# Performance work log

Hardware: AMD Instinct MI355X
Metric: run time of the kernel (lower is better)

The kernel has to match this reference:

```python
import jax, jax.numpy as jnp
import numpy as np

B, S, D, H = 2, 2048, 2048, 16
HD = D // H  # 128, head_dim (even, as asserted)
MAX_POS = 2048


def setup_inputs() -> dict:
    key = jax.random.key(0)
    ks = jax.random.split(key, 5)
    x = jax.random.normal(ks[0], (B, S, D), jnp.float32)
    Wq = jax.random.normal(ks[1], (D, D), jnp.float32) * 0.02
    Wk = jax.random.normal(ks[2], (D, D), jnp.float32) * 0.02
    Wv = jax.random.normal(ks[3], (D, D), jnp.float32) * 0.02
    Wo = jax.random.normal(ks[4], (D, D), jnp.float32) * 0.02
    # standard RoPE tables: [MAX_POS, HD]
    inv_freq = 1.0 / (10000.0 ** (jnp.arange(0, HD, 2, dtype=jnp.float32) / HD))
    angles = jnp.arange(MAX_POS, dtype=jnp.float32)[:, None] * inv_freq  # [P, HD/2]
    emb = jnp.concatenate([angles, angles], axis=-1)  # [P, HD]
    cos_freqs = jnp.cos(emb)
    sin_freqs = jnp.sin(emb)
    position_ids = jnp.broadcast_to(jnp.arange(S, dtype=jnp.int32), (B, S))
    return {"x": x, "cos_freqs": cos_freqs, "sin_freqs": sin_freqs,
            "Wq": Wq, "Wk": Wk, "Wv": Wv, "Wo": Wo,
            "position_ids": position_ids}


def _apply_rope(t, cos, sin, position_ids):
    # t: [b, s, h, hd]; cos/sin: [P, hd]; position_ids: [b, s]
    c = cos[position_ids][:, :, None, :]  # [b, s, 1, hd]
    s_ = sin[position_ids][:, :, None, :]
    t1, t2 = jnp.split(t, 2, axis=-1)
    rot = jnp.concatenate([-t2, t1], axis=-1)  # rotate-half
    return t * c + rot * s_


def reference(x, cos_freqs, sin_freqs, Wq, Wk, Wv, Wo, position_ids):
    b, s, d = x.shape
    q = (x @ Wq).reshape(b, s, H, HD)
    k = (x @ Wk).reshape(b, s, H, HD)  # n_kv_heads == n_heads
    v = (x @ Wv).reshape(b, s, H, HD)
    q = _apply_rope(q, cos_freqs, sin_freqs, position_ids)
    k = _apply_rope(k, cos_freqs, sin_freqs, position_ids)
    # [b, h, s, hd]
    q_t = jnp.swapaxes(q, 1, 2)
    k_t = jnp.swapaxes(k, 1, 2)
    v_t = jnp.swapaxes(v, 1, 2)
    scale = 1.0 / jnp.sqrt(jnp.float32(HD))
    scores = jnp.einsum('bhsd,bhtd->bhst', q_t, k_t) * scale  # O(s^2) matrix
    causal = jnp.tril(jnp.ones((s, s), dtype=bool))
    scores = jnp.where(causal[None, None, :, :], scores, -1e9)
    weights = jax.nn.softmax(scores, axis=-1)
    out = jnp.einsum('bhst,bhtd->bhsd', weights, v_t)
    out = jnp.swapaxes(out, 1, 2).reshape(b, s, d)
    out = out @ Wo
    return (out, k, v)  # kv_cache is post-RoPE, pre-transpose as in original
```

## Files before the change

kernel.cpp:

```cpp
#include <hip/hip_runtime.h>
#include <hip/hip_bf16.h>

#define B_ 2
#define S_ 2048
#define D_ 2048
#define H_ 16
#define HD_ 128
#define M_ (B_*S_)
#define BSD ((size_t)B_*S_*D_)

typedef short bf16x8 __attribute__((ext_vector_type(8)));
typedef float floatx4 __attribute__((ext_vector_type(4)));
typedef __hip_bfloat16 bf16;

union cv8 { bf16 h[8]; uint4 u; bf16x8 v; };

__device__ inline cv8 cvt8(const float4 a, const float4 b) {
    cv8 c;
    c.h[0] = __float2bfloat16(a.x); c.h[1] = __float2bfloat16(a.y);
    c.h[2] = __float2bfloat16(a.z); c.h[3] = __float2bfloat16(a.w);
    c.h[4] = __float2bfloat16(b.x); c.h[5] = __float2bfloat16(b.y);
    c.h[6] = __float2bfloat16(b.z); c.h[7] = __float2bfloat16(b.w);
    return c;
}

__device__ __forceinline__ void gld16(const void* g, void* l) {
    __builtin_amdgcn_global_load_lds(
        (const __attribute__((address_space(1))) unsigned int*)g,
        (__attribute__((address_space(3))) unsigned int*)l,
        16, 0, 0);
}

__global__ __launch_bounds__(256) void transpose_w(
    const float* __restrict__ W, bf16* __restrict__ Wt, int N, int K)
{
    __shared__ float T[32][33];
    const int k0 = blockIdx.x * 32, n0 = blockIdx.y * 32;
    const int r = threadIdx.x >> 3, c4 = (threadIdx.x & 7) * 4;
    float4 v = *(const float4*)&W[(size_t)(k0 + r) * N + n0 + c4];
    T[r][c4+0] = v.x; T[r][c4+1] = v.y; T[r][c4+2] = v.z; T[r][c4+3] = v.w;
    __syncthreads();
    union { bf16 h[4]; uint2 u; } o;
    #pragma unroll
    for (int i = 0; i < 4; ++i) o.h[i] = __float2bfloat16(T[c4 + i][r]);
    *(uint2*)&Wt[(size_t)(n0 + r) * K + k0 + c4] = o.u;
}

__global__ __launch_bounds__(256) void transpose_w_s(
    const float* __restrict__ W, bf16* __restrict__ Wt, int N, int K)
{
    __shared__ float T[32][33];
    const int k0 = blockIdx.x * 32, n0 = blockIdx.y * 32;
    const int r = threadIdx.x >> 3, c4 = (threadIdx.x & 7) * 4;
    float4 v = *(const float4*)&W[(size_t)(k0 + r) * N + n0 + c4];
    T[r][c4+0] = v.x; T[r][c4+1] = v.y; T[r][c4+2] = v.z; T[r][c4+3] = v.w;
    __syncthreads();
    union { bf16 h[4]; uint2 u; } o;
    #pragma unroll
    for (int i = 0; i < 4; ++i) o.h[i] = __float2bfloat16(T[c4 + i][r]);
    const int n = n0 + r;
    size_t bo = (size_t)n * (size_t)K * 2 + ((unsigned)((k0 + c4) * 2) ^ ((n & 3) << 4));
    *(uint2*)((char*)Wt + bo) = o.u;
}

__global__ __launch_bounds__(256) void pack_bf16(
    const float* __restrict__ src, bf16* __restrict__ dst)
{
    const size_t i = ((size_t)blockIdx.x * 256 + threadIdx.x) * 8;
    cv8 c = cvt8(*(const float4*)(src + i), *(const float4*)(src + i + 4));
    size_t bo = i * 2;
    bo ^= (size_t)(((bo >> 12) & 3) << 4);
    *(uint4*)((char*)dst + bo) = c.u;
}

__global__ __launch_bounds__(256) void rope_pack_k(
    float* __restrict__ k, bf16* __restrict__ kbb,
    const float* __restrict__ cf, const float* __restrict__ sf,
    const int* __restrict__ pos)
{
    const int idx = blockIdx.x * 256 + threadIdx.x;
    const int dg = idx & 7;
    const int h  = (idx >> 3) & (H_-1);
    const int bs = idx >> 7;
    const int s  = bs & (S_-1);
    const int b  = bs >> 11;
    const int p  = pos[bs];
    const size_t base = (size_t)bs * D_ + h*HD_ + dg*8;
    float lo[8], hi[8], c1[8], s1[8], c2[8], s2[8];
    *(float4*)&lo[0] = *(const float4*)&k[base];
    *(float4*)&lo[4] = *(const float4*)&k[base + 4];
    *(float4*)&hi[0] = *(const float4*)&k[base + 64];
    *(float4*)&hi[4] = *(const float4*)&k[base + 68];
    const float* cp = cf + (size_t)p*HD_ + dg*8;
    const float* sp = sf + (size_t)p*HD_ + dg*8;
    *(float4*)&c1[0] = *(const float4*)cp;        *(float4*)&c1[4] = *(const float4*)(cp + 4);
    *(float4*)&s1[0] = *(const float4*)sp;        *(float4*)&s1[4] = *(const float4*)(sp + 4);
    *(float4*)&c2[0] = *(const float4*)(cp + 64); *(float4*)&c2[4] = *(const float4*)(cp + 68);
    *(float4*)&s2[0] = *(const float4*)(sp + 64); *(float4*)&s2[4] = *(const float4*)(sp + 68);
    float nl[8], nh[8];
    #pragma unroll
    for (int j = 0; j < 8; ++j) {
        nl[j] = lo[j]*c1[j] - hi[j]*s1[j];
        nh[j] = hi[j]*c2[j] + lo[j]*s2[j];
    }
    *(float4*)&k[base]      = *(float4*)&nl[0];
    *(float4*)&k[base + 4]  = *(float4*)&nl[4];
    *(float4*)&k[base + 64] = *(float4*)&nh[0];
    *(float4*)&k[base + 68] = *(float4*)&nh[4];
    cv8 clo, chi;
    #pragma unroll
    for (int j = 0; j < 8; ++j) {
        clo.h[j] = __float2bfloat16(nl[j]);
        chi.h[j] = __float2bfloat16(nh[j]);
    }
    const size_t rowb = ((size_t)(b*H_ + h)*S_ + s) * (size_t)(HD_*2);
    *(uint4*)((char*)kbb + rowb + ((dg*16)       ^ ((s & 7) << 4))) = clo.u;
    *(uint4*)((char*)kbb + rowb + (((dg+8)*16)   ^ ((s & 7) << 4))) = chi.u;
}

__global__ __launch_bounds__(256) void pack_vt(
    const float* __restrict__ src, bf16* __restrict__ dst)
{
    __shared__ float T[32][33];
    const int s0 = blockIdx.x * 32;
    const int d0 = blockIdx.y * 32;
    const int bh = blockIdx.z;
    const int b = bh >> 4, h = bh & (H_-1);
    const int r = threadIdx.x >> 3, c4 = (threadIdx.x & 7) * 4;
    float4 v = *(const float4*)&src[((size_t)(b*S_ + s0 + r)*H_ + h)*HD_ + d0 + c4];
    T[r][c4+0] = v.x; T[r][c4+1] = v.y; T[r][c4+2] = v.z; T[r][c4+3] = v.w;
    __syncthreads();
    union { bf16 h4[4]; uint2 u; } o;
    #pragma unroll
    for (int i = 0; i < 4; ++i) o.h4[i] = __float2bfloat16(T[c4 + i][r]);
    const int hd = d0 + r;
    size_t rowb = ((size_t)bh*HD_ + hd) * (size_t)(S_*2);
    size_t colb = (size_t)(s0 + c4) * 2;
    colb = (colb & ~(size_t)127) | (((unsigned)colb & 127u) ^ (unsigned)((hd & 7) << 4));
    *(uint2*)((char*)dst + rowb + colb) = o.u;
}

__global__ __launch_bounds__(256, 3) void gemm_bb2(
    const bf16* __restrict__ A, const bf16* __restrict__ Wt,
    float* __restrict__ C, int M, int N, int K)
{
    __shared__ __align__(16) bf16 As[128][32];
    __shared__ __align__(16) bf16 Bs[128][32];
    const int nwg = (int)(gridDim.x * gridDim.y);
    int id = (int)(blockIdx.y * gridDim.x + blockIdx.x);
    if ((nwg & 7) == 0) id = (id & 7) * (nwg >> 3) + (id >> 3);
    const int m0 = (id % (int)gridDim.x) * 128;
    const int n0 = (id / (int)gridDim.x) * 128;
    const int tid = threadIdx.x, lane = tid & 63, w = tid >> 6;
    const int quad = lane >> 4, l16 = lane & 15;
    const int wrow = (w >> 1) * 64, wcol = (w & 1) * 64;
    const size_t K2 = (size_t)K * 2;

    floatx4 acc[4][4] = {};

    const char* Ab = (const char*)A;
    const char* Bb = (const char*)Wt;
    char* AsB = (char*)&As[0][0];
    char* BsB = (char*)&Bs[0][0];
    const int srow = lane >> 2;
    const int scol = (lane & 3) * 16;

    for (int kt = 0; kt < K; kt += 32) {
        #pragma unroll
        for (int j = 0; j < 2; ++j) {
            const int row = w*32 + j*16 + srow;
            gld16(Ab + (size_t)(m0 + row)*K2 + (size_t)(kt*2) + scol,
                  AsB + w*2048 + j*1024);
            gld16(Bb + (size_t)(n0 + row)*K2 + (size_t)(kt*2) + scol,
                  BsB + w*2048 + j*1024);
        }
        __syncthreads();

        bf16x8 af[4], bfr[4];
        #pragma unroll
        for (int t = 0; t < 4; ++t) {
            const int ra = wrow + t*16 + l16;
            af[t]  = *(const bf16x8*)(AsB + ra*64 + ((quad*16) ^ ((ra & 3) << 4)));
            const int rb = wcol + t*16 + l16;
            bfr[t] = *(const bf16x8*)(BsB + rb*64 + ((quad*16) ^ ((rb & 3) << 4)));
        }
        #pragma unroll
        for (int mt = 0; mt < 4; ++mt)
            #pragma unroll
            for (int nt = 0; nt < 4; ++nt)
                acc[mt][nt] = __builtin_amdgcn_mfma_f32_16x16x32_bf16(
                    af[mt], bfr[nt], acc[mt][nt], 0, 0, 0);
        __syncthreads();
    }

    #pragma unroll
    for (int mt = 0; mt < 4; ++mt)
        #pragma unroll
        for (int nt = 0; nt < 4; ++nt)
            #pragma unroll
            for (int r = 0; r < 4; ++r)
                C[(size_t)(m0 + wrow + mt*16 + quad*4 + r) * N
                  + n0 + wcol + nt*16 + l16] = acc[mt][nt][r];
}

__global__ __launch_bounds__(256) void gemm_xw(
    const float* __restrict__ A, const bf16* __restrict__ Wt,
    float* __restrict__ C, int M, int N, int K)
{
    __shared__ __align__(16) bf16 As[128][40];
    __shared__ __align__(16) bf16 Bs[128][40];
    const int m0 = blockIdx.x * 128, n0 = blockIdx.y * 128;
    const int tid = threadIdx.x, lane = tid & 63, w = tid >> 6;
    const int quad = lane >> 4, l16 = lane & 15;
    const int wrow = (w >> 1) * 64, wcol = (w & 1) * 64;
    floatx4 acc[4][4] = {};
    const int arow = tid >> 2;
    const int acol = (tid & 3) * 8;
    for (int kt = 0; kt < K; kt += 32) {
        #pragma unroll
        for (int p = 0; p < 2; ++p) {
            const int r = p*64 + arow;
            const float* ap = &A[(size_t)(m0 + r) * K + kt + acol];
            cv8 ca = cvt8(*(const float4*)ap, *(const float4*)(ap + 4));
            *(uint4*)&As[r][acol] = ca.u;
            const bf16* bp = &Wt[(size_t)(n0 + r) * K + kt + acol];
            *(uint4*)&Bs[r][acol] = *(const uint4*)bp;
        }
        __syncthreads();
        bf16x8 af[4], bfr[4];
        #pragma unroll
        for (int t = 0; t < 4; ++t) {
            af[t]  = *(const bf16x8*)&As[wrow + t*16 + l16][quad*8];
            bfr[t] = *(const bf16x8*)&Bs[wcol + t*16 + l16][quad*8];
        }
        #pragma unroll
        for (int mt = 0; mt < 4; ++mt)
            #pragma unroll
            for (int nt = 0; nt < 4; ++nt)
                acc[mt][nt] = __builtin_amdgcn_mfma_f32_16x16x32_bf16(
                    af[mt], bfr[nt], acc[mt][nt], 0, 0, 0);
        __syncthreads();
    }
    #pragma unroll
    for (int mt = 0; mt < 4; ++mt)
        #pragma unroll
        for (int nt = 0; nt < 4; ++nt)
            #pragma unroll
            for (int r = 0; r < 4; ++r)
                C[(size_t)(m0 + wrow + mt*16 + quad*4 + r) * N
                  + n0 + wcol + nt*16 + l16] = acc[mt][nt][r];
}

__global__ __launch_bounds__(256) void gemm_f32(
    const float* __restrict__ A, const float* __restrict__ W,
    float* __restrict__ C, int M, int N, int K)
{
    __shared__ __align__(16) bf16 As[64][40];
    __shared__ __align__(16) bf16 Bs[64][40];
    const int m0 = blockIdx.x * 64, n0 = blockIdx.y * 64;
    const int tid = threadIdx.x, lane = tid & 63, w = tid >> 6;
    const int quad = lane >> 4, l16 = lane & 15;
    const int wrow = (w >> 1) * 32, wcol = (w & 1) * 32;
    floatx4 acc[2][2] = {};
    const int ar = tid >> 2, ac = (tid & 3) * 8;
    const int br = tid >> 3, bc = (tid & 7) * 8;
    for (int kt = 0; kt < K; kt += 32) {
        {
            const float* ap = &A[(size_t)(m0 + ar) * K + kt + ac];
            cv8 c = cvt8(*(const float4*)ap, *(const float4*)(ap + 4));
            *(uint4*)&As[ar][ac] = c.u;
        }
        {
            const float* wp = &W[(size_t)(kt + br) * N + n0 + bc];
            cv8 c = cvt8(*(const float4*)wp, *(const float4*)(wp + 4));
            #pragma unroll
            for (int i = 0; i < 8; ++i) Bs[bc + i][br] = c.h[i];
        }
        __syncthreads();
        bf16x8 af[2], bfr[2];
        #pragma unroll
        for (int t = 0; t < 2; ++t) {
            af[t]  = *(const bf16x8*)&As[wrow + t*16 + l16][quad*8];
            bfr[t] = *(const bf16x8*)&Bs[wcol + t*16 + l16][quad*8];
        }
        #pragma unroll
        for (int mt = 0; mt < 2; ++mt)
            #pragma unroll
            for (int nt = 0; nt < 2; ++nt)
                acc[mt][nt] = __builtin_amdgcn_mfma_f32_16x16x32_bf16(
                    af[mt], bfr[nt], acc[mt][nt], 0, 0, 0);
        __syncthreads();
    }
    #pragma unroll
    for (int mt = 0; mt < 2; ++mt)
        #pragma unroll
        for (int nt = 0; nt < 2; ++nt)
            #pragma unroll
            for (int r = 0; r < 4; ++r)
                C[(size_t)(m0 + wrow + mt*16 + quad*4 + r) * N
                  + n0 + wcol + nt*16 + l16] = acc[mt][nt][r];
}

__global__ __launch_bounds__(256) void rope_kernel(
    float* __restrict__ q, float* __restrict__ k,
    const float* __restrict__ cf, const float* __restrict__ sf,
    const int* __restrict__ pos)
{
    const int PAIRS = B_*S_*H_*(HD_/2);
    int idx = blockIdx.x * 256 + threadIdx.x;
    float* t = q;
    if (idx >= PAIRS) { t = k; idx -= PAIRS; }
    const int d  = idx & 63;
    const int h  = (idx >> 6) & (H_-1);
    const int bs = idx >> 10;
    const int p  = pos[bs];
    const float c1 = cf[p*HD_ + d],      s1 = sf[p*HD_ + d];
    const float c2 = cf[p*HD_ + d + 64], s2 = sf[p*HD_ + d + 64];
    const size_t base = (size_t)bs * D_ + h*HD_ + d;
    const float t1 = t[base], t2 = t[base + 64];
    t[base]      = t1*c1 - t2*s1;
    t[base + 64] = t2*c2 + t1*s2;
}

__global__ __launch_bounds__(256, 3) void flash_attn_v6(
    const float* __restrict__ qg, const bf16* __restrict__ kb,
    const bf16* __restrict__ vb, bf16* __restrict__ ob,
    const float* __restrict__ cf, const float* __restrict__ sf,
    const int* __restrict__ pos)
{
    __shared__ __align__(16) bf16 Ks[2][64][128];
    __shared__ __align__(16) bf16 Vt[128][64];

    const int qi = (int)gridDim.x - 1 - (int)blockIdx.x;
    const int q0 = qi * 64;
    const int bh = blockIdx.y;
    const int b = bh >> 4, h = bh & (H_-1);
    const int tid = threadIdx.x, lane = tid & 63, w = tid >> 6;
    const int quad = lane >> 4, l16 = lane & 15;

    const char* kbase = (const char*)(kb + (size_t)bh * S_ * HD_);
    const char* vbase = (const char*)(vb + (size_t)bh * HD_ * S_);
    char* ksd = (char*)&Ks[0][0][0];
    char* vtd = (char*)&Vt[0][0];

    const int klofs = w*4096;
    const int vrow0 = w*32 + (lane >> 3);
    const int vcb   = (lane & 7) * 16;

    #pragma unroll
    for (int j = 0; j < 4; ++j)
        gld16(kbase + klofs + j*1024 + lane*16, ksd + klofs + j*1024);

    const int qrow = q0 + w*16 + l16;
    const float* qptr = qg + ((size_t)(b*S_ + qrow))*D_ + h*HD_;
    float rq[4][8];
    #pragma unroll
    for (int c = 0; c < 4; ++c) {
        const float* qp = qptr + c*32 + quad*8;
        *(float4*)&rq[c][0] = *(const float4*)qp;
        *(float4*)&rq[c][4] = *(const float4*)(qp + 4);
    }
    const int p = pos[b*S_ + qrow];
    bf16x8 qf[4];
    #pragma unroll
    for (int c = 0; c < 4; ++c) {
        const float* cp = cf + (size_t)p*HD_ + c*32 + quad*8;
        const float* sp = sf + (size_t)p*HD_ + c*32 + quad*8;
        float cc[8], ss[8];
        *(float4*)&cc[0] = *(const float4*)cp; *(float4*)&cc[4] = *(const float4*)(cp+4);
        *(float4*)&ss[0] = *(const float4*)sp; *(float4*)&ss[4] = *(const float4*)(sp+4);
        cv8 cv;
        #pragma unroll
        for (int j = 0; j < 8; ++j) {
            const float o = (c < 2) ? rq[c][j]*cc[j] - rq[c^2][j]*ss[j]
                                    : rq[c][j]*cc[j] + rq[c^2][j]*ss[j];
            cv.h[j] = __float2bfloat16(o);
        }
        qf[c] = cv.v;
    }

    floatx4 acc_o[8] = {};
    float m_run = -30000.0f, l_run = 0.0f;
    const int qr_sm = q0 + w*16 + l16;
    const float SCL = 0.08838834764831845f;

    __syncthreads();

    for (int kt = 0; kt <= qi; ++kt) {
        const int cur = kt & 1;
        const char* ksb = ksd + cur*16384;

        if (kt < qi) {
            const char* ksrc = kbase + (size_t)(kt+1)*16384;
            char* kdst = ksd + (cur^1)*16384;
            #pragma unroll
            for (int j = 0; j < 4; ++j)
                gld16(ksrc + klofs + j*1024 + lane*16, kdst + klofs + j*1024);
        }
        {
            const char* vsrc = vbase + (size_t)kt*128;
            #pragma unroll
            for (int j = 0; j < 4; ++j)
                gld16(vsrc + (size_t)(vrow0 + j*8)*(S_*2) + vcb,
                      vtd + w*4096 + j*1024);
        }

        floatx4 sc[4] = {};
        __builtin_amdgcn_s_setprio(1);
        #pragma unroll
        for (int c = 0; c < 4; ++c)
            #pragma unroll
            for (int kc = 0; kc < 4; ++kc) {
                bf16x8 kf = *(const bf16x8*)(ksb + (c*16 + l16)*256
                              + ((kc*64 + quad*16) ^ ((l16 & 7) << 4)));
                sc[c] = __builtin_amdgcn_mfma_f32_16x16x32_bf16(kf, qf[kc], sc[c], 0, 0, 0);
            }
        __builtin_amdgcn_s_setprio(0);

        const int k0 = kt * 64;
        float pv[4][4], mt = -30000.0f;
        #pragma unroll
        for (int c = 0; c < 4; ++c)
            #pragma unroll
            for (int r = 0; r < 4; ++r) {
                const int kcol = k0 + c*16 + quad*4 + r;
                float s = sc[c][r] * SCL;
                if (kcol > qr_sm) s = -30000.0f;
                pv[c][r] = s;
                mt = fmaxf(mt, s);
            }
        mt = fmaxf(mt, __shfl_xor(mt, 16, 64));
        mt = fmaxf(mt, __shfl_xor(mt, 32, 64));
        const float mn = fmaxf(m_run, mt);
        const float alpha = __expf(m_run - mn);
        m_run = mn;
        float sum = 0.0f;
        #pragma unroll
        for (int c = 0; c < 4; ++c)
            #pragma unroll
            for (int r = 0; r < 4; ++r) {
                pv[c][r] = __expf(pv[c][r] - mn);
                sum += pv[c][r];
            }
        sum += __shfl_xor(sum, 16, 64);
        sum += __shfl_xor(sum, 32, 64);
        l_run = l_run * alpha + sum;

        float at[4];
        #pragma unroll
        for (int r = 0; r < 4; ++r) at[r] = __shfl(alpha, quad*4 + r, 64);
        #pragma unroll
        for (int n = 0; n < 8; ++n)
            #pragma unroll
            for (int r = 0; r < 4; ++r)
                acc_o[n][r] *= at[r];

        unsigned pk[4][2];
        #pragma unroll
        for (int c = 0; c < 4; ++c) {
            union { bf16 h2[2]; unsigned u; } a0, a1;
            a0.h2[0] = __float2bfloat16(pv[c][0]); a0.h2[1] = __float2bfloat16(pv[c][1]);
            a1.h2[0] = __float2bfloat16(pv[c][2]); a1.h2[1] = __float2bfloat16(pv[c][3]);
            pk[c][0] = a0.u; pk[c][1] = a1.u;
        }
        bf16x8 pf[2];
        #pragma unroll
        for (int kc2 = 0; kc2 < 2; ++kc2) {
            union { unsigned u[4]; bf16x8 v; } wv;
            #pragma unroll
            for (int u_ = 0; u_ < 4; ++u_) {
                const int sl = ((quad & 1)*2 + (u_ >> 1))*16 + l16;
                const unsigned w0 = __shfl(pk[kc2*2 + 0][u_ & 1], sl, 64);
                const unsigned w1 = __shfl(pk[kc2*2 + 1][u_ & 1], sl, 64);
                wv.u[u_] = (quad >> 1) ? w1 : w0;
            }
            pf[kc2] = wv.v;
        }

        __syncthreads();

        __builtin_amdgcn_s_setprio(1);
        #pragma unroll
        for (int n = 0; n < 8; ++n)
            #pragma unroll
            for (int kc2 = 0; kc2 < 2; ++kc2) {
                bf16x8 vf = *(const bf16x8*)(vtd + (n*16 + l16)*128
                               + ((kc2*64 + quad*16) ^ ((l16 & 7) << 4)));
                acc_o[n] = __builtin_amdgcn_mfma_f32_16x16x32_bf16(pf[kc2], vf, acc_o[n], 0, 0, 0);
            }
        __builtin_amdgcn_s_setprio(0);

        __syncthreads();
    }

    const float linv = 1.0f / l_run;
    float lt[4];
    #pragma unroll
    for (int r = 0; r < 4; ++r) lt[r] = __shfl(linv, quad*4 + r, 64);
    #pragma unroll
    for (int n = 0; n < 8; ++n)
        #pragma unroll
        for (int r = 0; r < 4; ++r) {
            const int qr = q0 + w*16 + quad*4 + r;
            size_t bo = ((((size_t)(b*S_ + qr))*D_ + h*HD_ + n*16 + l16) * 2)
                        ^ (size_t)(r << 4);
            *(bf16*)((char*)ob + bo) = __float2bfloat16(acc_o[n][r] * lt[r]);
        }
}

__global__ __launch_bounds__(256) void flash_attn(
    const float* qg, const float* __restrict__ kg,
    const float* __restrict__ vg, float* og)
{
    __shared__ __align__(16) bf16 Ks[64][136];
    __shared__ __align__(16) bf16 Vt[128][72];
    __shared__ __align__(16) bf16 Ps[4][16][72];

    const int qi = (int)gridDim.x - 1 - (int)blockIdx.x;
    const int q0 = qi * 64;
    const int bh = blockIdx.y;
    const int b = bh >> 4, h = bh & (H_-1);
    const int tid = threadIdx.x, lane = tid & 63, w = tid >> 6;
    const int quad = lane >> 4, l16 = lane & 15;

    const int qrow = q0 + w*16 + l16;
    const float* qptr = qg + ((size_t)(b*S_ + qrow)*H_ + h)*HD_;
    bf16x8 qf[4];
    #pragma unroll
    for (int c = 0; c < 4; ++c) {
        const float* qp = qptr + c*32 + quad*8;
        cv8 cv = cvt8(*(const float4*)qp, *(const float4*)(qp + 4));
        qf[c] = cv.v;
    }

    floatx4 acc_o[8] = {};
    float m_run[4], l_run[4];
    #pragma unroll
    for (int r = 0; r < 4; ++r) { m_run[r] = -30000.0f; l_run[r] = 0.f; }

    const int ksr = tid >> 2, kscg = (tid & 3) * 32;
    const int vk2 = (tid & 31) * 2, vf8 = (tid >> 5) * 8;

    for (int kt = 0; kt <= qi; ++kt) {
        const int k0 = kt * 64;
        {
            const float* kp = kg + ((size_t)(b*S_ + k0 + ksr)*H_ + h)*HD_ + kscg;
            #pragma unroll
            for (int j = 0; j < 4; ++j) {
                cv8 c = cvt8(*(const float4*)(kp + j*8), *(const float4*)(kp + j*8 + 4));
                *(uint4*)&Ks[ksr][kscg + j*8] = c.u;
            }
        }
        {
            #pragma unroll
            for (int pq = 0; pq < 2; ++pq) {
                const int f = vf8 + pq*64;
                const float* v0p = vg + ((size_t)(b*S_ + k0 + vk2)*H_ + h)*HD_ + f;
                const float* v1p = v0p + D_;
                cv8 c0 = cvt8(*(const float4*)v0p, *(const float4*)(v0p + 4));
                cv8 c1 = cvt8(*(const float4*)v1p, *(const float4*)(v1p + 4));
                #pragma unroll
                for (int i = 0; i < 8; ++i) {
                    union { bf16 h2[2]; unsigned u; } pk;
                    pk.h2[0] = c0.h[i]; pk.h2[1] = c1.h[i];
                    *(unsigned*)&Vt[f + i][vk2] = pk.u;
                }
            }
        }
        __syncthreads();

        floatx4 sc[4] = {};
        #pragma unroll
        for (int c = 0; c < 4; ++c)
            #pragma unroll
            for (int kc = 0; kc < 4; ++kc) {
                bf16x8 kf = *(const bf16x8*)&Ks[c*16 + l16][kc*32 + quad*8];
                sc[c] = __builtin_amdgcn_mfma_f32_16x16x32_bf16(qf[kc], kf, sc[c], 0, 0, 0);
            }

        float pv[4][4], mt_[4];
        #pragma unroll
        for (int r = 0; r < 4; ++r) mt_[r] = -30000.0f;
        #pragma unroll
        for (int c = 0; c < 4; ++c) {
            const int kcol = k0 + c*16 + l16;
            #pragma unroll
            for (int r = 0; r < 4; ++r) {
                const int qr = q0 + w*16 + quad*4 + r;
                float s = sc[c][r] * 0.08838834764831845f;
                if (kcol > qr) s = -30000.0f;
                pv[c][r] = s;
                mt_[r] = fmaxf(mt_[r], s);
            }
        }
        #pragma unroll
        for (int off = 1; off < 16; off <<= 1)
            #pragma unroll
            for (int r = 0; r < 4; ++r)
                mt_[r] = fmaxf(mt_[r], __shfl_xor(mt_[r], off, 64));
        float alpha[4];
        #pragma unroll
        for (int r = 0; r < 4; ++r) {
            float mn = fmaxf(m_run[r], mt_[r]);
            alpha[r] = __expf(m_run[r] - mn);
            m_run[r] = mn;
        }
        #pragma unroll
        for (int c = 0; c < 4; ++c)
            #pragma unroll
            for (int r = 0; r < 4; ++r)
                pv[c][r] = __expf(pv[c][r] - m_run[r]);
        #pragma unroll
        for (int r = 0; r < 4; ++r) {
            float s = pv[0][r] + pv[1][r] + pv[2][r] + pv[3][r];
            #pragma unroll
            for (int off = 1; off < 16; off <<= 1)
                s += __shfl_xor(s, off, 64);
            l_run[r] = l_run[r] * alpha[r] + s;
        }
        #pragma unroll
        for (int c = 0; c < 4; ++c)
            #pragma unroll
            for (int r = 0; r < 4; ++r)
                Ps[w][quad*4 + r][c*16 + l16] = __float2bfloat16(pv[c][r]);
        __syncthreads();

        #pragma unroll
        for (int n = 0; n < 8; ++n)
            #pragma unroll
            for (int r = 0; r < 4; ++r)
                acc_o[n][r] *= alpha[r];
        bf16x8 pf[2];
        #pragma unroll
        for (int kc2 = 0; kc2 < 2; ++kc2)
            pf[kc2] = *(const bf16x8*)&Ps[w][l16][kc2*32 + quad*8];
        #pragma unroll
        for (int n = 0; n < 8; ++n)
            #pragma unroll
            for (int kc2 = 0; kc2 < 2; ++kc2) {
                bf16x8 vf = *(const bf16x8*)&Vt[n*16 + l16][kc2*32 + quad*8];
                acc_o[n] = __builtin_amdgcn_mfma_f32_16x16x32_bf16(pf[kc2], vf, acc_o[n], 0, 0, 0);
            }
        __syncthreads();
    }

    #pragma unroll
    for (int n = 0; n < 8; ++n)
        #pragma unroll
        for (int r = 0; r < 4; ++r) {
            const int qr = q0 + w*16 + quad*4 + r;
            og[((size_t)(b*S_ + qr))*D_ + h*HD_ + n*16 + l16] = acc_o[n][r] / l_run[r];
        }
}

extern "C" void kernel_launch(void* const* d_in, const int* in_sizes, int n_in,
                              void* d_out, int out_size, void* d_ws, size_t ws_size,
                              hipStream_t stream) {
    const float* x  = (const float*)d_in[0];
    const float* cf = (const float*)d_in[1];
    const float* sf = (const float*)d_in[2];
    const float* Wq = (const float*)d_in[3];
    const float* Wk = (const float*)d_in[4];
    const float* Wv = (const float*)d_in[5];
    const float* Wo = (const float*)d_in[6];
    const int*  pos = (const int*)d_in[7];

    float* out  = (float*)d_out;
    float* kout = out + BSD;
    float* vout = out + 2*BSD;

    const size_t WT_BYTES = (size_t)D_ * D_ * sizeof(bf16);
    const size_t TB_BYTES = BSD * sizeof(bf16);
    const size_t NEED_V6  = WT_BYTES + 4 * TB_BYTES;
    const bool big = ws_size >= WT_BYTES + (size_t)128 * D_ * sizeof(float);

    if (ws_size >= NEED_V6) {
        bf16* wt  = (bf16*)d_ws;
        bf16* xb  = wt + (size_t)D_ * D_;
        bf16* kbb = xb + BSD;
        bf16* vbb = kbb + BSD;
        bf16* obb = vbb + BSD;

        dim3 tg(D_/32, D_/32), gg(M_/128, D_/128);
        pack_bf16<<<(int)(BSD/8/256), 256, 0, stream>>>(x, xb);
        transpose_w_s<<<tg, 256, 0, stream>>>(Wq, wt, D_, D_);
        gemm_bb2<<<gg, 256, 0, stream>>>(xb, wt, out,  M_, D_, D_);
        transpose_w_s<<<tg, 256, 0, stream>>>(Wk, wt, D_, D_);
        gemm_bb2<<<gg, 256, 0, stream>>>(xb, wt, kout, M_, D_, D_);
        transpose_w_s<<<tg, 256, 0, stream>>>(Wv, wt, D_, D_);
        gemm_bb2<<<gg, 256, 0, stream>>>(xb, wt, vout, M_, D_, D_);
        rope_pack_k<<<(B_*S_*H_*8)/256, 256, 0, stream>>>(kout, kbb, cf, sf, pos);
        pack_vt<<<dim3(S_/32, HD_/32, B_*H_), 256, 0, stream>>>(vout, vbb);
        flash_attn_v6<<<dim3(S_/64, B_*H_), 256, 0, stream>>>(out, kbb, vbb, obb,
                                                              cf, sf, pos);
        transpose_w_s<<<tg, 256, 0, stream>>>(Wo, wt, D_, D_);
        gemm_bb2<<<gg, 256, 0, stream>>>(obb, wt, out, M_, D_, D_);
    } else if (big) {
        bf16*  wt  = (bf16*)d_ws;
        float* cws = (float*)((char*)d_ws + WT_BYTES);
        const size_t crem = ws_size - WT_BYTES;
        dim3 tg(D_/32, D_/32), gg(M_/128, D_/128);
        transpose_w<<<tg, 256, 0, stream>>>(Wq, wt, D_, D_);
        gemm_xw<<<gg, 256, 0, stream>>>(x, wt, out,  M_, D_, D_);
        transpose_w<<<tg, 256, 0, stream>>>(Wk, wt, D_, D_);
        gemm_xw<<<gg, 256, 0, stream>>>(x, wt, kout, M_, D_, D_);
        transpose_w<<<tg, 256, 0, stream>>>(Wv, wt, D_, D_);
        gemm_xw<<<gg, 256, 0, stream>>>(x, wt, vout, M_, D_, D_);
        rope_kernel<<<(2*B_*S_*H_*(HD_/2))/256, 256, 0, stream>>>(out, kout, cf, sf, pos);
        flash_attn<<<dim3(S_/64, B_*H_), 256, 0, stream>>>(out, kout, vout, out);
        transpose_w<<<tg, 256, 0, stream>>>(Wo, wt, D_, D_);
        int R = 128;
        while (R < M_ && (size_t)(2*R) * D_ * sizeof(float) <= crem) R *= 2;
        for (int m0 = 0; m0 < M_; m0 += R) {
            gemm_xw<<<dim3(R/128, D_/128), 256, 0, stream>>>(out + (size_t)m0*D_, wt, cws, R, D_, D_);
            hipMemcpyAsync(out + (size_t)m0*D_, cws, (size_t)R*D_*sizeof(float),
                           hipMemcpyDeviceToDevice, stream);
        }
    } else {
        float* wsb = (float*)d_ws;
        dim3 gg(M_/64, D_/64);
        gemm_f32<<<gg, 256, 0, stream>>>(x, Wq, out,  M_, D_, D_);
        gemm_f32<<<gg, 256, 0, stream>>>(x, Wk, kout, M_, D_, D_);
        gemm_f32<<<gg, 256, 0, stream>>>(x, Wv, vout, M_, D_, D_);
        rope_kernel<<<(2*B_*S_*H_*(HD_/2))/256, 256, 0, stream>>>(out, kout, cf, sf, pos);
        flash_attn<<<dim3(S_/64, B_*H_), 256, 0, stream>>>(out, kout, vout, out);
        int R = 64;
        while (R < M_ && (size_t)(2*R) * D_ * sizeof(float) <= ws_size) R *= 2;
        if ((size_t)R * D_ * sizeof(float) > ws_size) R = 64;
        for (int m0 = 0; m0 < M_; m0 += R) {
            gemm_f32<<<dim3(R/64, D_/64), 256, 0, stream>>>(out + (size_t)m0*D_, Wo, wsb, R, D_, D_);
            hipMemcpyAsync(out + (size_t)m0*D_, wsb, (size_t)R*D_*sizeof(float),
                           hipMemcpyDeviceToDevice, stream);
        }
    }
}
```

Measured before the change: 557.1 us.

## Fuse Q/K/V projections into one concatenated-weight GEMM launch

The three weights are transposed into one contiguous [3D, D] bf16 buffer, and a single gemm_qkv launch with a 3x wider N grid computes Q, K and V. Each tile routes its output to the matching Q/K/V slab by N index. This removes two GEMM launches and the tail effects between them, giving one larger grid that fills the GPU better. In exchange it needs more workspace for three weight copies, and it reuses the xb buffer for the attention output to fit.

Result: faster. 532.3 us (-4.4%).

```diff
diff --git a/kernel.cpp b/kernel.cpp
--- a/kernel.cpp
+++ b/kernel.cpp
@@ -140,6 +140,71 @@
     *(uint2*)((char*)dst + rowb + colb) = o.u;
 }
 
+__global__ __launch_bounds__(256, 3) void gemm_qkv(
+    const bf16* __restrict__ A, const bf16* __restrict__ Wt,
+    float* __restrict__ C, int M, int K)
+{
+    __shared__ __align__(16) bf16 As[128][32];
+    __shared__ __align__(16) bf16 Bs[128][32];
+    const int nwg = (int)(gridDim.x * gridDim.y);
+    int id = (int)(blockIdx.y * gridDim.x + blockIdx.x);
+    if ((nwg & 7) == 0) id = (id & 7) * (nwg >> 3) + (id >> 3);
+    const int m0  = (id % (int)gridDim.x) * 128;
+    const int n0g = (id / (int)gridDim.x) * 128;
+    float* Cb = C + (size_t)(n0g >> 11) * BSD;
+    const int n0 = n0g & 2047;
+    const int tid = threadIdx.x, lane = tid & 63, w = tid >> 6;
+    const int quad = lane >> 4, l16 = lane & 15;
+    const int wrow = (w >> 1) * 64, wcol = (w & 1) * 64;
+    const size_t K2 = (size_t)K * 2;
+
+    floatx4 acc[4][4] = {};
+
+    const char* Ab = (const char*)A;
+    const char* Bb = (const char*)Wt;
+    char* AsB = (char*)&As[0][0];
+    char* BsB = (char*)&Bs[0][0];
+    const int srow = lane >> 2;
+    const int scol = (lane & 3) * 16;
+
+    for (int kt = 0; kt < K; kt += 32) {
+        #pragma unroll
+        for (int j = 0; j < 2; ++j) {
+            const int row = w*32 + j*16 + srow;
+            gld16(Ab + (size_t)(m0 + row)*K2 + (size_t)(kt*2) + scol,
+                  AsB + w*2048 + j*1024);
+            gld16(Bb + (size_t)(n0g + row)*K2 + (size_t)(kt*2) + scol,
+                  BsB + w*2048 + j*1024);
+        }
+        __syncthreads();
+
+        bf16x8 af[4], bfr[4];
+        #pragma unroll
+        for (int t = 0; t < 4; ++t) {
+            const int ra = wrow + t*16 + l16;
+            af[t]  = *(const bf16x8*)(AsB + ra*64 + ((quad*16) ^ ((ra & 3) << 4)));
+            const int rb = wcol + t*16 + l16;
+            bfr[t] = *(const bf16x8*)(BsB + rb*64 + ((quad*16) ^ ((rb & 3) << 4)));
+        }
+        #pragma unroll
+        for (int mt = 0; mt < 4; ++mt)
+            #pragma unroll
+            for (int nt = 0; nt < 4; ++nt)
+                acc[mt][nt] = __builtin_amdgcn_mfma_f32_16x16x32_bf16(
+                    af[mt], bfr[nt], acc[mt][nt], 0, 0, 0);
+        __syncthreads();
+    }
+
+    #pragma unroll
+    for (int mt = 0; mt < 4; ++mt)
+        #pragma unroll
+        for (int nt = 0; nt < 4; ++nt)
+            #pragma unroll
+            for (int r = 0; r < 4; ++r)
+                Cb[(size_t)(m0 + wrow + mt*16 + quad*4 + r) * 2048
+                   + n0 + wcol + nt*16 + l16] = acc[mt][nt][r];
+}
+
 __global__ __launch_bounds__(256, 3) void gemm_bb2(
     const bf16* __restrict__ A, const bf16* __restrict__ Wt,
     float* __restrict__ C, int M, int N, int K)
@@ -669,32 +734,31 @@
     float* kout = out + BSD;
     float* vout = out + 2*BSD;
 
-    const size_t WT_BYTES = (size_t)D_ * D_ * sizeof(bf16);
+    const size_t D2 = (size_t)D_ * D_;
+    const size_t WT_BYTES = D2 * sizeof(bf16);
     const size_t TB_BYTES = BSD * sizeof(bf16);
-    const size_t NEED_V6  = WT_BYTES + 4 * TB_BYTES;
+    const size_t NEED_V7  = 3*WT_BYTES + 3*TB_BYTES;
     const bool big = ws_size >= WT_BYTES + (size_t)128 * D_ * sizeof(float);
 
-    if (ws_size >= NEED_V6) {
-        bf16* wt  = (bf16*)d_ws;
-        bf16* xb  = wt + (size_t)D_ * D_;
+    if (ws_size >= NEED_V7) {
+        bf16* wt3 = (bf16*)d_ws;
+        bf16* xb  = wt3 + 3*D2;
         bf16* kbb = xb + BSD;
         bf16* vbb = kbb + BSD;
-        bf16* obb = vbb + BSD;
-
-        dim3 tg(D_/32, D_/32), gg(M_/128, D_/128);
+        bf16* obb = xb;
+
+        dim3 tg(D_/32, D_/32);
         pack_bf16<<<(int)(BSD/8/256), 256, 0, stream>>>(x, xb);
-        transpose_w_s<<<tg, 256, 0, stream>>>(Wq, wt, D_, D_);
-        gemm_bb2<<<gg, 256, 0, stream>>>(xb, wt, out,  M_, D_, D_);
-        transpose_w_s<<<tg, 256, 0, stream>>>(Wk, wt, D_, D_);
-        gemm_bb2<<<gg, 256, 0, stream>>>(xb, wt, kout, M_, D_, D_);
-        transpose_w_s<<<tg, 256, 0, stream>>>(Wv, wt, D_, D_);
-        gemm_bb2<<<gg, 256, 0, stream>>>(xb, wt, vout, M_, D_, D_);
+        transpose_w_s<<<tg, 256, 0, stream>>>(Wq, wt3,        D_, D_);
+        transpose_w_s<<<tg, 256, 0, stream>>>(Wk, wt3 + D2,   D_, D_);
+        transpose_w_s<<<tg, 256, 0, stream>>>(Wv, wt3 + 2*D2, D_, D_);
+        gemm_qkv<<<dim3(M_/128, (3*D_)/128), 256, 0, stream>>>(xb, wt3, out, M_, D_);
         rope_pack_k<<<(B_*S_*H_*8)/256, 256, 0, stream>>>(kout, kbb, cf, sf, pos);
         pack_vt<<<dim3(S_/32, HD_/32, B_*H_), 256, 0, stream>>>(vout, vbb);
         flash_attn_v6<<<dim3(S_/64, B_*H_), 256, 0, stream>>>(out, kbb, vbb, obb,
                                                               cf, sf, pos);
-        transpose_w_s<<<tg, 256, 0, stream>>>(Wo, wt, D_, D_);
-        gemm_bb2<<<gg, 256, 0, stream>>>(obb, wt, out, M_, D_, D_);
+        transpose_w_s<<<tg, 256, 0, stream>>>(Wo, wt3, D_, D_);
+        gemm_bb2<<<dim3(M_/128, D_/128), 256, 0, stream>>>(obb, wt3, out, M_, D_, D_);
     } else if (big) {
         bf16*  wt  = (bf16*)d_ws;
         float* cws = (float*)((char*)d_ws + WT_BYTES);
```
